# Kernel tuning notes

Hardware: AMD Instinct MI355X
Metric: run time of the kernel (lower is better)

Reference implementation:

```python
import jax, jax.numpy as jnp
import numpy as np

B, S, DM = 2, 2048, 1024
H, DH = 16, 64
SCALE = jnp.sqrt(jnp.float32(DH))  # dot_scale = sqrt(dim_head)


def setup_inputs() -> dict:
    key = jax.random.key(0)
    ks = jax.random.split(key, 9)
    std = 1.0 / np.sqrt(DM)
    x = jax.random.normal(ks[0], (B, S, DM), dtype=jnp.float32)
    Wq = jax.random.uniform(ks[1], (DM, DM), jnp.float32, -std, std)
    bq = jax.random.uniform(ks[2], (DM,), jnp.float32, -std, std)
    Wk = jax.random.uniform(ks[3], (DM, DM), jnp.float32, -std, std)
    bk = jax.random.uniform(ks[4], (DM,), jnp.float32, -std, std)
    Wv = jax.random.uniform(ks[5], (DM, DM), jnp.float32, -std, std)
    bv = jax.random.uniform(ks[6], (DM,), jnp.float32, -std, std)
    Wo = jax.random.uniform(ks[7], (DM, DM), jnp.float32, -std, std)
    bo = jax.random.uniform(ks[8], (DM,), jnp.float32, -std, std)
    # causal mask: 1 = masked (future positions), broadcast over batch
    causal = jnp.triu(jnp.ones((S, S), dtype=jnp.int32), k=1)
    attention_mask = jnp.broadcast_to(causal, (B, S, S))
    return {"x": x, "Wq": Wq, "bq": bq, "Wk": Wk, "bk": bk,
            "Wv": Wv, "bv": bv, "Wo": Wo, "bo": bo,
            "attention_mask": attention_mask}


def reference(x, Wq, bq, Wk, bk, Wv, bv, Wo, bo, attention_mask):
    # Linear layers (torch nn.Linear: y = x @ W^T + b)
    q = (x @ Wq.T + bq).reshape(B, S, H, DH).transpose(0, 2, 1, 3)  # (B,H,S,DH)
    k = (x @ Wk.T + bk).reshape(B, S, H, DH).transpose(0, 2, 1, 3)  # (B,H,S,DH)
    v = (x @ Wv.T + bv).reshape(B, S, H, DH).transpose(0, 2, 1, 3)  # (B,H,S,DH)
    # scores: (B,H,S,S), then mask==1 -> -inf, softmax over last dim
    scores = jnp.einsum('bhsd,bhtd->bhst', q, k) / SCALE
    mask = attention_mask[:, None, :, :]  # (B,1,S,S)
    scores = jnp.where(mask == 1, -jnp.inf, scores)
    attn = jax.nn.softmax(scores, axis=-1)
    # dropout is identity in eval mode
    ctx = jnp.einsum('bhst,bhtd->bshd', attn, v).reshape(B, S, H * DH)
    return ctx @ Wo.T + bo
```

## Files before the change

### kernel.cpp

```cpp
#include <hip/hip_runtime.h>
#include <stdint.h>

typedef unsigned short u16;
typedef __attribute__((ext_vector_type(8))) short bf16x8;
typedef __attribute__((ext_vector_type(4))) float f32x4;

#define BATCH 2
#define S_LEN 2048
#define DMODEL 1024
#define NH 16
#define DHEAD 64
#define MTOT 4096
#define QSCALE 0.18033688011112042f

#define GL2LDS(g, l) \
  __builtin_amdgcn_global_load_lds((const __attribute__((address_space(1))) void*)(g), \
                                   (__attribute__((address_space(3))) void*)(l), 16, 0, 0)

__device__ __forceinline__ u16 f2bf(float x) {
  union { float f; uint32_t u; } v; v.f = x;
  uint32_t r = v.u + 0x7fffu + ((v.u >> 16) & 1u);
  return (u16)(r >> 16);
}
__device__ __forceinline__ u16 f2bf_fast(float x) {
  union { float f; uint32_t u; } v; v.f = x;
  return (u16)((v.u + 0x8000u) >> 16);
}

struct CvtArgs {
  const float* src[5];
  u16* dst[5];
};

__global__ __launch_bounds__(256) void cvt_all(CvtArgs a) {
  int bx = blockIdx.x;
  int region, off;
  if (bx < 4096) { region = 0; off = bx; }
  else { region = 1 + ((bx - 4096) >> 10); off = (bx - 4096) & 1023; }
  const float* s = a.src[region];
  u16* d = a.dst[region];
  int i = (off * 256 + threadIdx.x) * 4;
  float4 v = *(const float4*)(s + i);
  uint2 pk;
  pk.x = (uint32_t)f2bf(v.x) | ((uint32_t)f2bf(v.y) << 16);
  pk.y = (uint32_t)f2bf(v.z) | ((uint32_t)f2bf(v.w) << 16);
  *(uint2*)(d + i) = pk;
}

__device__ __forceinline__ void gemm_body(const u16* __restrict__ A,
                                          const u16* __restrict__ W,
                                          const float* __restrict__ bias,
                                          void* __restrict__ out,
                                          int mode, float scale) {
  __shared__ u16 As[128 * 32];
  __shared__ u16 Bs[128 * 32];
  const int tid = threadIdx.x;
  const int m0 = blockIdx.y * 128;
  const int n0 = blockIdx.x * 128;
  const int wave = tid >> 6, lane = tid & 63;
  const int wm = (wave >> 1) * 64, wn = (wave & 1) * 64;
  const int quad = lane >> 4, l15 = lane & 15;

  const int row0 = tid >> 2, g0 = ((tid & 3) ^ (row0 & 3)) * 8;
  const int row1 = (tid + 256) >> 2, g1 = ((tid & 3) ^ (row1 & 3)) * 8;
  const int lb0 = wave * 512;
  const int lb1 = 2048 + wave * 512;
  const int xk = (quad ^ (l15 & 3)) * 8;

  f32x4 acc[4][4] = {};

  for (int kt = 0; kt < DMODEL; kt += 32) {
    GL2LDS(A + (size_t)(m0 + row0) * DMODEL + kt + g0, As + lb0);
    GL2LDS(A + (size_t)(m0 + row1) * DMODEL + kt + g1, As + lb1);
    GL2LDS(W + (size_t)(n0 + row0) * DMODEL + kt + g0, Bs + lb0);
    GL2LDS(W + (size_t)(n0 + row1) * DMODEL + kt + g1, Bs + lb1);
    __syncthreads();
    bf16x8 af[4], bfr[4];
#pragma unroll
    for (int bi = 0; bi < 4; ++bi)
      af[bi] = *(const bf16x8*)(&As[(wm + bi * 16 + l15) * 32 + xk]);
#pragma unroll
    for (int bj = 0; bj < 4; ++bj)
      bfr[bj] = *(const bf16x8*)(&Bs[(wn + bj * 16 + l15) * 32 + xk]);
#pragma unroll
    for (int bi = 0; bi < 4; ++bi)
#pragma unroll
      for (int bj = 0; bj < 4; ++bj)
        acc[bi][bj] = __builtin_amdgcn_mfma_f32_16x16x32_bf16(af[bi], bfr[bj], acc[bi][bj], 0, 0, 0);
    __syncthreads();
  }

#pragma unroll
  for (int bi = 0; bi < 4; ++bi) {
#pragma unroll
    for (int bj = 0; bj < 4; ++bj) {
      int n = n0 + wn + bj * 16 + l15;
      float bval = bias[n];
#pragma unroll
      for (int r = 0; r < 4; ++r) {
        int m = m0 + wm + bi * 16 + quad * 4 + r;
        float v = (acc[bi][bj][r] + bval) * scale;
        u16 bvu = f2bf(v);
        int b = m >> 11, s = m & 2047;
        int h = n >> 6, d = n & 63;
        size_t bh = (size_t)(b * NH + h);
        if (mode == 1)
          ((u16*)out)[(bh * S_LEN + s) * DHEAD + d] = bvu;
        else
          ((u16*)out)[((bh * 256 + (s >> 3)) * 64 + d) * 8 + (s & 7)] = bvu;
      }
    }
  }
}

struct QKVArgs {
  const u16* w[3];
  const float* b[3];
  u16* o[3];
};

__global__ __launch_bounds__(256) void qkv_gemm(const u16* __restrict__ xb, QKVArgs a) {
  int z = blockIdx.z;
  int mode = (z == 2) ? 2 : 1;
  float scale = (z == 0) ? QSCALE : 1.0f;
  gemm_body(xb, a.w[z], a.b[z], a.o[z], mode, scale);
}

__global__ __launch_bounds__(256) void out_gemm(const u16* __restrict__ A,
                                                const u16* __restrict__ W,
                                                const float* __restrict__ bias,
                                                float* __restrict__ out) {
  __shared__ u16 As[128 * 32];
  __shared__ u16 Bs[64 * 32];
  const int tid = threadIdx.x;
  const int m0 = blockIdx.y * 128;
  const int n0 = blockIdx.x * 64;
  const int wave = tid >> 6, lane = tid & 63;
  const int wm = (wave >> 1) * 64, wn = (wave & 1) * 32;
  const int quad = lane >> 4, l15 = lane & 15;

  const int row0 = tid >> 2, g0 = ((tid & 3) ^ (row0 & 3)) * 8;
  const int row1 = (tid + 256) >> 2, g1 = ((tid & 3) ^ (row1 & 3)) * 8;
  const int lb0 = wave * 512;
  const int lb1 = 2048 + wave * 512;
  const int xk = (quad ^ (l15 & 3)) * 8;

  f32x4 acc[4][2] = {};

  for (int kt = 0; kt < DMODEL; kt += 32) {
    GL2LDS(A + (size_t)(m0 + row0) * DMODEL + kt + g0, As + lb0);
    GL2LDS(A + (size_t)(m0 + row1) * DMODEL + kt + g1, As + lb1);
    GL2LDS(W + (size_t)(n0 + row0) * DMODEL + kt + g0, Bs + lb0);
    __syncthreads();
    bf16x8 af[4], bfr[2];
#pragma unroll
    for (int bi = 0; bi < 4; ++bi)
      af[bi] = *(const bf16x8*)(&As[(wm + bi * 16 + l15) * 32 + xk]);
#pragma unroll
    for (int bj = 0; bj < 2; ++bj)
      bfr[bj] = *(const bf16x8*)(&Bs[(wn + bj * 16 + l15) * 32 + xk]);
#pragma unroll
    for (int bi = 0; bi < 4; ++bi)
#pragma unroll
      for (int bj = 0; bj < 2; ++bj)
        acc[bi][bj] = __builtin_amdgcn_mfma_f32_16x16x32_bf16(af[bi], bfr[bj], acc[bi][bj], 0, 0, 0);
    __syncthreads();
  }

#pragma unroll
  for (int bi = 0; bi < 4; ++bi) {
#pragma unroll
    for (int bj = 0; bj < 2; ++bj) {
      int n = n0 + wn + bj * 16 + l15;
      float bval = bias[n];
#pragma unroll
      for (int r = 0; r < 4; ++r) {
        int m = m0 + wm + bi * 16 + quad * 4 + r;
        out[(size_t)m * DMODEL + n] = acc[bi][bj][r] + bval;
      }
    }
  }
}

__global__ __launch_bounds__(256, 4) void attn(const u16* __restrict__ Q,
                                               const u16* __restrict__ Kg,
                                               const u16* __restrict__ Vt8,
                                               u16* __restrict__ ctx,
                                               float* __restrict__ part_o,
                                               float* __restrict__ part_l) {
  __shared__ u16 Kd[2][64 * 64];
  __shared__ u16 Vd[2][64 * 64];
  __shared__ u16 Ps[64 * 64];
  const int tid = threadIdx.x;
  const int qp = blockIdx.x >> 6;
  const int hh = (blockIdx.x >> 5) & 1;
  const int bh = blockIdx.x & 31;
  const int wave = tid >> 6, lane = tid & 63;
  const int quad = lane >> 4, l15 = lane & 15;
  const size_t base = (size_t)bh * S_LEN * DHEAD;
  const int b = bh >> 4, h = bh & 15;
  const int xk7 = l15 & 7;
  const int pidx = qp * 32 + bh;

#define STAGE(kt_, pb)                                                                   \
  do {                                                                                   \
    _Pragma("unroll")                                                                    \
    for (int i_ = 0; i_ < 2; ++i_) {                                                     \
      int c_ = tid + 256 * i_;                                                           \
      int row_ = c_ >> 3, g_ = ((c_ & 7) ^ (row_ & 7)) * 8;                              \
      GL2LDS(Kg + base + (size_t)((kt_) * 64 + row_) * 64 + g_,                          \
             &Kd[pb][0] + i_ * 2048 + wave * 512);                                       \
      GL2LDS(Vt8 + base + (size_t)((kt_) * 512 + c_) * 8,                                \
             &Vd[pb][0] + i_ * 2048 + wave * 512);                                       \
    }                                                                                    \
  } while (0)

  const int nph = hh ? 1 : 2;
  for (int ph = 0; ph < nph; ++ph) {
    int qt, k0, k1, pmode;
    if (hh == 0 && ph == 0) { qt = qp;      k0 = 0;       k1 = qp;      pmode = 0; }
    else if (hh == 0)       { qt = 31 - qp; k0 = 0;       k1 = 15 - qp; pmode = 1; }
    else                    { qt = 31 - qp; k0 = 16 - qp; k1 = 31 - qp; pmode = 1; }

    const int qrow = qt * 64 + wave * 16 + l15;
    bf16x8 qf0 = *(const bf16x8*)(Q + base + (size_t)qrow * DHEAD + quad * 8);
    bf16x8 qf1 = *(const bf16x8*)(Q + base + (size_t)qrow * DHEAD + 32 + quad * 8);

    float l_part[4] = {0.f, 0.f, 0.f, 0.f};
    f32x4 o[4] = {};

    STAGE(k0, 0);

    for (int kt = k0; kt <= k1; ++kt) {
      const int p = (kt - k0) & 1;
      __syncthreads();
      if (kt < k1) STAGE(kt + 1, p ^ 1);

      const bool diag = (kt == qt);
      f32x4 s_acc[4];
#pragma unroll
      for (int bj = 0; bj < 4; ++bj) {
        if (diag && bj > wave) {
          s_acc[bj] = f32x4{-1e30f, -1e30f, -1e30f, -1e30f};
          continue;
        }
        const int krow = (bj * 16 + l15) * 64;
        bf16x8 kf0 = *(const bf16x8*)(&Kd[p][krow + ((quad ^ xk7) * 8)]);
        bf16x8 kf1 = *(const bf16x8*)(&Kd[p][krow + (((quad + 4) ^ xk7) * 8)]);
        f32x4 t = {0.f, 0.f, 0.f, 0.f};
        t = __builtin_amdgcn_mfma_f32_16x16x32_bf16(qf0, kf0, t, 0, 0, 0);
        t = __builtin_amdgcn_mfma_f32_16x16x32_bf16(qf1, kf1, t, 0, 0, 0);
        s_acc[bj] = t;
      }

      if (diag) {
#pragma unroll
        for (int bj = 0; bj < 4; ++bj) {
          int kg = kt * 64 + bj * 16 + l15;
#pragma unroll
          for (int r = 0; r < 4; ++r) {
            int qg = qt * 64 + wave * 16 + quad * 4 + r;
            if (kg > qg) s_acc[bj][r] = -1e30f;
          }
        }
      }

#pragma unroll
      for (int bj = 0; bj < 4; ++bj) {
#pragma unroll
        for (int r = 0; r < 4; ++r) {
          float pv = exp2f(s_acc[bj][r]);
          l_part[r] += pv;
          int row = wave * 16 + quad * 4 + r;
          int ch = (bj * 2 + (l15 >> 3)) ^ (row & 7);
          Ps[row * 64 + ch * 8 + (l15 & 7)] = f2bf_fast(pv);
        }
      }

      {
        const int row2 = wave * 16 + l15;
#pragma unroll
        for (int kk = 0; kk < 2; ++kk) {
          bf16x8 pf = *(const bf16x8*)(&Ps[row2 * 64 + (((kk << 2) + quad) ^ xk7) * 8]);
#pragma unroll
          for (int dj = 0; dj < 4; ++dj) {
            bf16x8 vf = *(const bf16x8*)(&Vd[p][((kk * 4 + quad) * 64 + dj * 16 + l15) * 8]);
            o[dj] = __builtin_amdgcn_mfma_f32_16x16x32_bf16(pf, vf, o[dj], 0, 0, 0);
          }
        }
      }
    }

    __syncthreads();

#pragma unroll
    for (int r = 0; r < 4; ++r) {
      float s = l_part[r];
      s += __shfl_xor(s, 1, 64);
      s += __shfl_xor(s, 2, 64);
      s += __shfl_xor(s, 4, 64);
      s += __shfl_xor(s, 8, 64);
      int row = wave * 16 + quad * 4 + r;
      if (pmode == 0) {
        float inv = 1.0f / s;
        int srow = qt * 64 + row;
        size_t rowbase = ((size_t)b * S_LEN + srow) * DMODEL + h * DHEAD;
#pragma unroll
        for (int dj = 0; dj < 4; ++dj)
          ctx[rowbase + dj * 16 + l15] = f2bf(o[dj][r] * inv);
      } else {
        float* po = part_o + ((size_t)hh * 512 + pidx) * 4096 + (size_t)row * 64;
#pragma unroll
        for (int dj = 0; dj < 4; ++dj)
          po[dj * 16 + l15] = o[dj][r];
        if (l15 == 0) part_l[((size_t)hh * 512 + pidx) * 64 + row] = s;
      }
    }
  }
#undef STAGE
}

__global__ __launch_bounds__(256) void combine(const float* __restrict__ part_o,
                                               const float* __restrict__ part_l,
                                               u16* __restrict__ ctx) {
  const int pidx = blockIdx.x;
  const int qp = pidx >> 5, bh = pidx & 31;
  const int qt = 31 - qp;
  const int b = bh >> 4, h = bh & 15;
  const float* poA = part_o + (size_t)pidx * 4096;
  const float* poB = part_o + (512 + (size_t)pidx) * 4096;
  const float* plA = part_l + (size_t)pidx * 64;
  const float* plB = part_l + (512 + (size_t)pidx) * 64;
  for (int i = threadIdx.x * 4; i < 4096; i += 1024) {
    int row = i >> 6, col = i & 63;
    float4 oa = *(const float4*)(poA + i);
    float4 ob = *(const float4*)(poB + i);
    float inv = 1.0f / (plA[row] + plB[row]);
    uint2 pk;
    pk.x = (uint32_t)f2bf((oa.x + ob.x) * inv) | ((uint32_t)f2bf((oa.y + ob.y) * inv) << 16);
    pk.y = (uint32_t)f2bf((oa.z + ob.z) * inv) | ((uint32_t)f2bf((oa.w + ob.w) * inv) << 16);
    int srow = qt * 64 + row;
    *(uint2*)(ctx + ((size_t)b * S_LEN + srow) * DMODEL + h * DHEAD + col) = pk;
  }
}

extern "C" void kernel_launch(void* const* d_in, const int* in_sizes, int n_in,
                              void* d_out, int out_size, void* d_ws, size_t ws_size,
                              hipStream_t stream) {
  const float* x  = (const float*)d_in[0];
  const float* Wq = (const float*)d_in[1];
  const float* bq = (const float*)d_in[2];
  const float* Wk = (const float*)d_in[3];
  const float* bk = (const float*)d_in[4];
  const float* Wv = (const float*)d_in[5];
  const float* bv = (const float*)d_in[6];
  const float* Wo = (const float*)d_in[7];
  const float* bo = (const float*)d_in[8];
  float* out = (float*)d_out;

  char* ws = (char*)d_ws;
  const size_t MB = 1u << 20;
  u16* xb   = (u16*)(ws + 0);
  u16* ctxb = xb;
  u16* wqb  = (u16*)(ws + 8 * MB);
  u16* wkb  = (u16*)(ws + 10 * MB);
  u16* wvb  = (u16*)(ws + 12 * MB);
  u16* wob  = (u16*)(ws + 14 * MB);
  u16* qb   = (u16*)(ws + 16 * MB);
  u16* kb   = (u16*)(ws + 24 * MB);
  u16* vtb  = (u16*)(ws + 32 * MB);
  float* part_o = (float*)d_out;
  float* part_l = (float*)(ws + 8 * MB);

  CvtArgs c;
  c.src[0] = x;  c.dst[0] = xb;
  c.src[1] = Wq; c.dst[1] = wqb;
  c.src[2] = Wk; c.dst[2] = wkb;
  c.src[3] = Wv; c.dst[3] = wvb;
  c.src[4] = Wo; c.dst[4] = wob;
  cvt_all<<<4096 + 4 * 1024, 256, 0, stream>>>(c);

  QKVArgs a;
  a.w[0] = wqb; a.w[1] = wkb; a.w[2] = wvb;
  a.b[0] = bq;  a.b[1] = bk;  a.b[2] = bv;
  a.o[0] = qb;  a.o[1] = kb;  a.o[2] = vtb;
  qkv_gemm<<<dim3(DMODEL / 128, MTOT / 128, 3), 256, 0, stream>>>(xb, a);

  attn<<<1024, 256, 0, stream>>>(qb, kb, vtb, ctxb, part_o, part_l);

  combine<<<512, 256, 0, stream>>>(part_o, part_l, ctxb);

  out_gemm<<<dim3(DMODEL / 64, MTOT / 128), 256, 0, stream>>>(ctxb, wob, bo, out);
}
```

Measured before the change: 214.5 us.

## Restructure attention to 128-row query tiles with 32x32 MFMA and split-K wave sets

The attention kernel now uses 512-thread blocks covering 128 query rows, with two sets of four waves that each take alternate key tiles and then reduce their partial outputs through LDS. Scores and PV products use 32x32x16 MFMA instead of 16x16x32. Probabilities stay in registers, rearranged with cross-lane shuffles rather than staged through LDS, and are packed with the hardware bf16 convert. The intent is more reuse per staged K/V tile, fewer LDS round trips and fewer instructions. The cost is higher register pressure, an extra intra-block reduction, and coarser work partitioning with only 512 blocks.

Result: slower. 224.0 us (+4.4%).

```diff
diff --git a/kernel.cpp b/kernel.cpp
--- a/kernel.cpp
+++ b/kernel.cpp
@@ -4,6 +4,8 @@
 typedef unsigned short u16;
 typedef __attribute__((ext_vector_type(8))) short bf16x8;
 typedef __attribute__((ext_vector_type(4))) float f32x4;
+typedef __attribute__((ext_vector_type(16))) float f32x16;
+typedef __attribute__((ext_vector_type(4))) uint32_t u32x4;
 
 #define BATCH 2
 #define S_LEN 2048
@@ -22,9 +24,11 @@
   uint32_t r = v.u + 0x7fffu + ((v.u >> 16) & 1u);
   return (u16)(r >> 16);
 }
-__device__ __forceinline__ u16 f2bf_fast(float x) {
-  union { float f; uint32_t u; } v; v.f = x;
-  return (u16)((v.u + 0x8000u) >> 16);
+
+__device__ __forceinline__ uint32_t cvtpk_bf16(float lo, float hi) {
+  uint32_t r;
+  asm("v_cvt_pk_bf16_f32 %0, %1, %2" : "=v"(r) : "v"(lo), "v"(hi));
+  return r;
 }
 
 struct CvtArgs {
@@ -182,140 +186,174 @@
   }
 }
 
-__global__ __launch_bounds__(256, 4) void attn(const u16* __restrict__ Q,
+__global__ __launch_bounds__(512, 4) void attn(const u16* __restrict__ Q,
                                                const u16* __restrict__ Kg,
                                                const u16* __restrict__ Vt8,
                                                u16* __restrict__ ctx,
                                                float* __restrict__ part_o,
                                                float* __restrict__ part_l) {
-  __shared__ u16 Kd[2][64 * 64];
-  __shared__ u16 Vd[2][64 * 64];
-  __shared__ u16 Ps[64 * 64];
+  __shared__ u16 Kd[4][64 * 64];
+  __shared__ u16 Vd[4][64 * 64];
   const int tid = threadIdx.x;
-  const int qp = blockIdx.x >> 6;
+  const int u = blockIdx.x >> 6;
   const int hh = (blockIdx.x >> 5) & 1;
   const int bh = blockIdx.x & 31;
   const int wave = tid >> 6, lane = tid & 63;
-  const int quad = lane >> 4, l15 = lane & 15;
+  const int set = wave >> 2, w4 = wave & 3;
+  const int l31 = lane & 31, hi = lane >> 5;
   const size_t base = (size_t)bh * S_LEN * DHEAD;
   const int b = bh >> 4, h = bh & 15;
-  const int xk7 = l15 & 7;
-  const int pidx = qp * 32 + bh;
-
-#define STAGE(kt_, pb)                                                                   \
-  do {                                                                                   \
-    _Pragma("unroll")                                                                    \
-    for (int i_ = 0; i_ < 2; ++i_) {                                                     \
-      int c_ = tid + 256 * i_;                                                           \
-      int row_ = c_ >> 3, g_ = ((c_ & 7) ^ (row_ & 7)) * 8;                              \
-      GL2LDS(Kg + base + (size_t)((kt_) * 64 + row_) * 64 + g_,                          \
-             &Kd[pb][0] + i_ * 2048 + wave * 512);                                       \
-      GL2LDS(Vt8 + base + (size_t)((kt_) * 512 + c_) * 8,                                \
-             &Vd[pb][0] + i_ * 2048 + wave * 512);                                       \
-    }                                                                                    \
+
+  const int srow_ = tid >> 3;
+  const int sg_ = ((tid & 7) ^ (srow_ & 7)) * 8;
+  const int sdst = wave * 512;
+
+#define STAGE(j_, jp_)                                                              \
+  do {                                                                              \
+    int t0_ = 2 * (j_);                                                             \
+    _Pragma("unroll")                                                               \
+    for (int i_ = 0; i_ < 2; ++i_) {                                                \
+      int t_ = t0_ + i_;                                                            \
+      if (t_ < nk) {                                                                \
+        int kt_ = k0 + t_;                                                          \
+        GL2LDS(Kg + base + (size_t)(kt_ * 64 + srow_) * 64 + sg_,                   \
+               &Kd[(jp_) * 2 + i_][0] + sdst);                                      \
+        GL2LDS(Vt8 + base + (size_t)(kt_ * 512 + tid) * 8,                          \
+               &Vd[(jp_) * 2 + i_][0] + sdst);                                      \
+      }                                                                             \
+    }                                                                               \
   } while (0)
 
   const int nph = hh ? 1 : 2;
   for (int ph = 0; ph < nph; ++ph) {
-    int qt, k0, k1, pmode;
-    if (hh == 0 && ph == 0) { qt = qp;      k0 = 0;       k1 = qp;      pmode = 0; }
-    else if (hh == 0)       { qt = 31 - qp; k0 = 0;       k1 = 15 - qp; pmode = 1; }
-    else                    { qt = 31 - qp; k0 = 16 - qp; k1 = 31 - qp; pmode = 1; }
-
-    const int qrow = qt * 64 + wave * 16 + l15;
-    bf16x8 qf0 = *(const bf16x8*)(Q + base + (size_t)qrow * DHEAD + quad * 8);
-    bf16x8 qf1 = *(const bf16x8*)(Q + base + (size_t)qrow * DHEAD + 32 + quad * 8);
-
-    float l_part[4] = {0.f, 0.f, 0.f, 0.f};
-    f32x4 o[4] = {};
-
-    STAGE(k0, 0);
-
-    for (int kt = k0; kt <= k1; ++kt) {
-      const int p = (kt - k0) & 1;
+    int qs, k0, nk, pmode, slot;
+    if (hh == 0 && ph == 0) { qs = u;      k0 = 0;          nk = 2 * u + 2;  pmode = 0; slot = 0; }
+    else if (hh == 0)       { qs = 15 - u; k0 = 0;          nk = 15 - 2 * u; pmode = 1; slot = u * 32 + bh; }
+    else                    { qs = 15 - u; k0 = 15 - 2 * u; nk = 17;         pmode = 1; slot = 256 + u * 32 + bh; }
+
+    const int q0 = qs * 128 + w4 * 32;
+    bf16x8 qf[4];
+#pragma unroll
+    for (int s = 0; s < 4; ++s)
+      qf[s] = *(const bf16x8*)(Q + base + (size_t)(q0 + l31) * DHEAD + s * 16 + hi * 8);
+
+    f32x16 o0 = {}, o1 = {};
+    float lp = 0.f;
+
+    const int jmax = (nk + 1) >> 1;
+    STAGE(0, 0);
+    for (int j = 0; j < jmax; ++j) {
+      const int jp = j & 1;
       __syncthreads();
-      if (kt < k1) STAGE(kt + 1, p ^ 1);
-
-      const bool diag = (kt == qt);
-      f32x4 s_acc[4];
-#pragma unroll
-      for (int bj = 0; bj < 4; ++bj) {
-        if (diag && bj > wave) {
-          s_acc[bj] = f32x4{-1e30f, -1e30f, -1e30f, -1e30f};
-          continue;
-        }
-        const int krow = (bj * 16 + l15) * 64;
-        bf16x8 kf0 = *(const bf16x8*)(&Kd[p][krow + ((quad ^ xk7) * 8)]);
-        bf16x8 kf1 = *(const bf16x8*)(&Kd[p][krow + (((quad + 4) ^ xk7) * 8)]);
-        f32x4 t = {0.f, 0.f, 0.f, 0.f};
-        t = __builtin_amdgcn_mfma_f32_16x16x32_bf16(qf0, kf0, t, 0, 0, 0);
-        t = __builtin_amdgcn_mfma_f32_16x16x32_bf16(qf1, kf1, t, 0, 0, 0);
-        s_acc[bj] = t;
-      }
-
-      if (diag) {
-#pragma unroll
-        for (int bj = 0; bj < 4; ++bj) {
-          int kg = kt * 64 + bj * 16 + l15;
-#pragma unroll
-          for (int r = 0; r < 4; ++r) {
-            int qg = qt * 64 + wave * 16 + quad * 4 + r;
-            if (kg > qg) s_acc[bj][r] = -1e30f;
+      if (j + 1 < jmax) STAGE(j + 1, jp ^ 1);
+      const int t = 2 * j + set;
+      if (t < nk) {
+        const int kt = k0 + t;
+        const int kb0 = kt * 64;
+        if (kb0 <= q0 + 31) {
+          const u16* Kt = &Kd[jp * 2 + set][0];
+          const u16* Vt = &Vd[jp * 2 + set][0];
+          f32x16 sa0 = {}, sa1 = {};
+#pragma unroll
+          for (int s = 0; s < 4; ++s) {
+            bf16x8 kf0 = *(const bf16x8*)(&Kt[l31 * 64 + ((((s * 2 + hi) ^ (l31 & 7))) * 8)]);
+            sa0 = __builtin_amdgcn_mfma_f32_32x32x16_bf16(kf0, qf[s], sa0, 0, 0, 0);
+          }
+#pragma unroll
+          for (int s = 0; s < 4; ++s) {
+            bf16x8 kf1 = *(const bf16x8*)(&Kt[(32 + l31) * 64 + ((((s * 2 + hi) ^ (l31 & 7))) * 8)]);
+            sa1 = __builtin_amdgcn_mfma_f32_32x32x16_bf16(kf1, qf[s], sa1, 0, 0, 0);
+          }
+          if (kb0 + 63 > q0) {
+            const int qg = q0 + l31;
+#pragma unroll
+            for (int r = 0; r < 16; ++r) {
+              int kg = kb0 + (r & 3) + 4 * hi + 8 * (r >> 2);
+              if (kg > qg) sa0[r] = -1e30f;
+              if (kg + 32 > qg) sa1[r] = -1e30f;
+            }
+          }
+          float p0[16], p1[16];
+#pragma unroll
+          for (int r = 0; r < 16; ++r) { p0[r] = exp2f(sa0[r]); lp += p0[r]; }
+#pragma unroll
+          for (int r = 0; r < 16; ++r) { p1[r] = exp2f(sa1[r]); lp += p1[r]; }
+          uint32_t P2[2][8];
+#pragma unroll
+          for (int m = 0; m < 8; ++m) {
+            P2[0][m] = cvtpk_bf16(p0[2 * m], p0[2 * m + 1]);
+            P2[1][m] = cvtpk_bf16(p1[2 * m], p1[2 * m + 1]);
+          }
+#pragma unroll
+          for (int n = 0; n < 4; ++n) {
+            const int kb = n >> 1, mb = 4 * (n & 1);
+            uint32_t A0 = P2[kb][mb], A0p = P2[kb][mb + 1];
+            uint32_t A1 = P2[kb][mb + 2], A1p = P2[kb][mb + 3];
+            uint32_t X0  = (uint32_t)__shfl_xor((int)A0, 32, 64);
+            uint32_t X0p = (uint32_t)__shfl_xor((int)A0p, 32, 64);
+            uint32_t X1  = (uint32_t)__shfl_xor((int)A1, 32, 64);
+            uint32_t X1p = (uint32_t)__shfl_xor((int)A1p, 32, 64);
+            u32x4 pw;
+            pw.x = hi ? X1 : A0;
+            pw.y = hi ? X1p : A0p;
+            pw.z = hi ? A1 : X0;
+            pw.w = hi ? A1p : X0p;
+            bf16x8 pfv = __builtin_bit_cast(bf16x8, pw);
+            bf16x8 vf0 = *(const bf16x8*)(&Vt[((2 * n + hi) * 64 + l31) * 8]);
+            bf16x8 vf1 = *(const bf16x8*)(&Vt[((2 * n + hi) * 64 + 32 + l31) * 8]);
+            o0 = __builtin_amdgcn_mfma_f32_32x32x16_bf16(pfv, vf0, o0, 0, 0, 0);
+            o1 = __builtin_amdgcn_mfma_f32_32x32x16_bf16(pfv, vf1, o1, 0, 0, 0);
           }
         }
       }
-
-#pragma unroll
-      for (int bj = 0; bj < 4; ++bj) {
-#pragma unroll
-        for (int r = 0; r < 4; ++r) {
-          float pv = exp2f(s_acc[bj][r]);
-          l_part[r] += pv;
-          int row = wave * 16 + quad * 4 + r;
-          int ch = (bj * 2 + (l15 >> 3)) ^ (row & 7);
-          Ps[row * 64 + ch * 8 + (l15 & 7)] = f2bf_fast(pv);
+    }
+    __syncthreads();
+
+    lp += __shfl_xor(lp, 32, 64);
+
+    float* Om = (float*)&Kd[0][0];
+    float* Ls = (float*)&Vd[0][0];
+    if (set == 1) {
+#pragma unroll
+      for (int r = 0; r < 16; ++r) {
+        int row = w4 * 32 + (r & 3) + 4 * hi + 8 * (r >> 2);
+        Om[row * 64 + l31] = o0[r];
+        Om[row * 64 + 32 + l31] = o1[r];
+      }
+      if (hi == 0) Ls[w4 * 32 + l31] = lp;
+    }
+    __syncthreads();
+    if (set == 0) {
+      lp += Ls[w4 * 32 + l31];
+#pragma unroll
+      for (int r = 0; r < 16; ++r) {
+        int row = w4 * 32 + (r & 3) + 4 * hi + 8 * (r >> 2);
+        o0[r] += Om[row * 64 + l31];
+        o1[r] += Om[row * 64 + 32 + l31];
+      }
+      if (pmode == 0) {
+        float inv = 1.0f / lp;
+#pragma unroll
+        for (int r = 0; r < 16; ++r) {
+          int rl = (r & 3) + 4 * hi + 8 * (r >> 2);
+          float invr = __shfl(inv, rl, 64);
+          int q = q0 + rl;
+          size_t rb = ((size_t)b * S_LEN + q) * DMODEL + h * DHEAD;
+          ctx[rb + l31] = f2bf(o0[r] * invr);
+          ctx[rb + 32 + l31] = f2bf(o1[r] * invr);
         }
-      }
-
-      {
-        const int row2 = wave * 16 + l15;
-#pragma unroll
-        for (int kk = 0; kk < 2; ++kk) {
-          bf16x8 pf = *(const bf16x8*)(&Ps[row2 * 64 + (((kk << 2) + quad) ^ xk7) * 8]);
-#pragma unroll
-          for (int dj = 0; dj < 4; ++dj) {
-            bf16x8 vf = *(const bf16x8*)(&Vd[p][((kk * 4 + quad) * 64 + dj * 16 + l15) * 8]);
-            o[dj] = __builtin_amdgcn_mfma_f32_16x16x32_bf16(pf, vf, o[dj], 0, 0, 0);
-          }
+      } else {
+        float* po = part_o + (size_t)slot * 8192 + (size_t)w4 * 32 * 64;
+#pragma unroll
+        for (int r = 0; r < 16; ++r) {
+          int rl = (r & 3) + 4 * hi + 8 * (r >> 2);
+          po[rl * 64 + l31] = o0[r];
+          po[rl * 64 + 32 + l31] = o1[r];
         }
+        if (hi == 0) part_l[slot * 128 + w4 * 32 + l31] = lp;
       }
     }
-
-    __syncthreads();
-
-#pragma unroll
-    for (int r = 0; r < 4; ++r) {
-      float s = l_part[r];
-      s += __shfl_xor(s, 1, 64);
-      s += __shfl_xor(s, 2, 64);
-      s += __shfl_xor(s, 4, 64);
-      s += __shfl_xor(s, 8, 64);
-      int row = wave * 16 + quad * 4 + r;
-      if (pmode == 0) {
-        float inv = 1.0f / s;
-        int srow = qt * 64 + row;
-        size_t rowbase = ((size_t)b * S_LEN + srow) * DMODEL + h * DHEAD;
-#pragma unroll
-        for (int dj = 0; dj < 4; ++dj)
-          ctx[rowbase + dj * 16 + l15] = f2bf(o[dj][r] * inv);
-      } else {
-        float* po = part_o + ((size_t)hh * 512 + pidx) * 4096 + (size_t)row * 64;
-#pragma unroll
-        for (int dj = 0; dj < 4; ++dj)
-          po[dj * 16 + l15] = o[dj][r];
-        if (l15 == 0) part_l[((size_t)hh * 512 + pidx) * 64 + row] = s;
-      }
-    }
+    __syncthreads();
   }
 #undef STAGE
 }
@@ -324,14 +362,14 @@
                                                const float* __restrict__ part_l,
                                                u16* __restrict__ ctx) {
   const int pidx = blockIdx.x;
-  const int qp = pidx >> 5, bh = pidx & 31;
-  const int qt = 31 - qp;
+  const int u = pidx >> 5, bh = pidx & 31;
+  const int qs = 15 - u;
   const int b = bh >> 4, h = bh & 15;
-  const float* poA = part_o + (size_t)pidx * 4096;
-  const float* poB = part_o + (512 + (size_t)pidx) * 4096;
-  const float* plA = part_l + (size_t)pidx * 64;
-  const float* plB = part_l + (512 + (size_t)pidx) * 64;
-  for (int i = threadIdx.x * 4; i < 4096; i += 1024) {
+  const float* poA = part_o + (size_t)pidx * 8192;
+  const float* poB = part_o + (size_t)(256 + pidx) * 8192;
+  const float* plA = part_l + pidx * 128;
+  const float* plB = part_l + (256 + pidx) * 128;
+  for (int i = threadIdx.x * 4; i < 8192; i += 1024) {
     int row = i >> 6, col = i & 63;
     float4 oa = *(const float4*)(poA + i);
     float4 ob = *(const float4*)(poB + i);
@@ -339,7 +377,7 @@
     uint2 pk;
     pk.x = (uint32_t)f2bf((oa.x + ob.x) * inv) | ((uint32_t)f2bf((oa.y + ob.y) * inv) << 16);
     pk.y = (uint32_t)f2bf((oa.z + ob.z) * inv) | ((uint32_t)f2bf((oa.w + ob.w) * inv) << 16);
-    int srow = qt * 64 + row;
+    int srow = qs * 128 + row;
     *(uint2*)(ctx + ((size_t)b * S_LEN + srow) * DMODEL + h * DHEAD + col) = pk;
   }
 }
@@ -386,9 +424,9 @@
   a.o[0] = qb;  a.o[1] = kb;  a.o[2] = vtb;
   qkv_gemm<<<dim3(DMODEL / 128, MTOT / 128, 3), 256, 0, stream>>>(xb, a);
 
-  attn<<<1024, 256, 0, stream>>>(qb, kb, vtb, ctxb, part_o, part_l);
-
-  combine<<<512, 256, 0, stream>>>(part_o, part_l, ctxb);
+  attn<<<512, 512, 0, stream>>>(qb, kb, vtb, ctxb, part_o, part_l);
+
+  combine<<<256, 256, 0, stream>>>(part_o, part_l, ctxb);
 
   out_gemm<<<dim3(DMODEL / 64, MTOT / 128), 256, 0, stream>>>(ctxb, wob, bo, out);
 }
```
